# Optimization experiments

Measured on AMD Instinct MI355X. Metric: run time of the kernel, lower is better.

The kernel has to match this reference:

```python
import jax, jax.numpy as jnp
import numpy as np

B, N, E, D, H = 8, 5000, 160000, 64, 128  # batch, nodes, edges, gnn hidden, head hidden


def _w(key, shape, scale=0.05):
    return jax.random.normal(key, shape, jnp.float32) * scale


def setup_inputs() -> dict:
    key = jax.random.key(0)
    ks = jax.random.split(key, 24)
    inp = {
        "x": jax.random.normal(ks[0], (B, N), jnp.float32),
        "edges": jax.random.randint(ks[1], (E, 2), 0, N, dtype=jnp.int32),
        "emb": _w(ks[2], (N, D)),
        # conv1: prepare FFN (2 layers, no bias, elu), update FFN (2 layers, bias)
        "c1_pw1": _w(ks[3], (D, D)), "c1_pw2": _w(ks[4], (D, D)),
        "c1_uw1": _w(ks[5], (2 * D, D)), "c1_ub1": jnp.zeros((D,), jnp.float32),
        "c1_uw2": _w(ks[6], (D, D)), "c1_ub2": jnp.zeros((D,), jnp.float32),
        # conv2
        "c2_pw1": _w(ks[7], (D, D)), "c2_pw2": _w(ks[8], (D, D)),
        "c2_uw1": _w(ks[9], (2 * D, D)), "c2_ub1": jnp.zeros((D,), jnp.float32),
        "c2_uw2": _w(ks[10], (D, D)), "c2_ub2": jnp.zeros((D,), jnp.float32),
        # TARnet prob heads: flatten -> Dense(H, elu) -> Dense(2) (mu, log_sigma)
        "w0a": _w(ks[11], (N * D, H), 0.005), "b0a": jnp.zeros((H,), jnp.float32),
        "w0b": _w(ks[12], (H, 2)), "b0b": jnp.zeros((2,), jnp.float32),
        "w1a": _w(ks[13], (N * D, H), 0.005), "b1a": jnp.zeros((H,), jnp.float32),
        "w1b": _w(ks[14], (H, 2)), "b1b": jnp.zeros((2,), jnp.float32),
    }
    return inp


def _graph_conv(h, edges, pw1, pw2, uw1, ub1, uw2, ub2):
    # h: [B, N, D]; edges: [E, 2] (parent, node)
    parents = jnp.take(h, edges[:, 0], axis=1)            # [B, E, D] gather
    m = jax.nn.elu(parents @ pw1)                          # prepare FFN (no bias)
    m = jax.nn.elu(m @ pw2)
    agg = jnp.zeros_like(h).at[:, edges[:, 1]].add(m)      # unsorted_segment_sum -> [B, N, D]
    hcat = jnp.concatenate([h, agg], axis=-1)              # combination_type='concat'
    u = jax.nn.elu(hcat @ uw1 + ub1)                       # update FFN
    return u @ uw2 + ub2                                   # final_activation=None


def reference(x, edges, emb,
              c1_pw1, c1_pw2, c1_uw1, c1_ub1, c1_uw2, c1_ub2,
              c2_pw1, c2_pw2, c2_uw1, c2_ub1, c2_uw2, c2_ub2,
              w0a, b0a, w0b, b0b, w1a, b1a, w1b, b1b):
    # node features scale learned per-node embeddings -> [B, N, D]
    h = x[:, :, None] * emb[None, :, :]
    h = _graph_conv(h, edges, c1_pw1, c1_pw2, c1_uw1, c1_ub1, c1_uw2, c1_ub2)
    h = _graph_conv(h, edges, c2_pw1, c2_pw2, c2_uw1, c2_ub1, c2_uw2, c2_ub2)
    phi = h.reshape(h.shape[0], -1)                        # flatten [B, N*D]
    y0 = jax.nn.elu(phi @ w0a + b0a) @ w0b + b0b           # [B, 2] (mu, log_sigma)
    y1 = jax.nn.elu(phi @ w1a + b1a) @ w1b + b1b           # [B, 2]
    return jnp.concatenate([y0, y1], axis=1)               # [B, 4]
```

## Files before the change

### kernel.cpp

```cpp
#include <hip/hip_runtime.h>


constexpr int B = 8, N = 5000, E = 160000, D = 64, H = 128;
constexpr int BN = B * N;
constexpr int ND = N * D;
constexpr long BND = (long)BN * D;
constexpr int KC = 320;
constexpr int NIT = KC / 8;
constexpr int XB = ND / KC;

using f32x4 = __attribute__((ext_vector_type(4))) float;

__device__ __forceinline__ float elu_f(float x) {
    return x > 0.0f ? x : __expf(x) - 1.0f;
}

__device__ __forceinline__ void g2lds16(const float* g, float* l) {
    __builtin_amdgcn_global_load_lds(
        (const __attribute__((address_space(1))) void*)g,
        (__attribute__((address_space(3))) void*)l, 16, 0, 0);
}

__global__ __launch_bounds__(256) void k_count(const int* __restrict__ edges,
                                               int* __restrict__ cnt) {
    int i = blockIdx.x * 256 + threadIdx.x;
    if (i < E) atomicAdd(&cnt[edges[2 * i + 1]], 1);
}

__global__ __launch_bounds__(256) void k_scan(const int* __restrict__ cnt,
                                              int* __restrict__ offs) {
    __shared__ int part[256];
    int t = threadIdx.x;
    const int CH = 20;
    int base = t * CH;
    int s = 0;
    for (int i = 0; i < CH; ++i) { int idx = base + i; if (idx < N) s += cnt[idx]; }
    part[t] = s;
    __syncthreads();
    for (int off = 1; off < 256; off <<= 1) {
        int add = (t >= off) ? part[t - off] : 0;
        __syncthreads();
        part[t] += add;
        __syncthreads();
    }
    int run = part[t] - s;
    for (int i = 0; i < CH; ++i) {
        int idx = base + i;
        if (idx < N) { offs[idx] = run; run += cnt[idx]; }
    }
    if (t == 255) offs[N] = run;
}

__global__ __launch_bounds__(256) void k_fill(const int* __restrict__ edges,
                                              const int* __restrict__ offs,
                                              int* __restrict__ cursor,
                                              int* __restrict__ elist) {
    int i = blockIdx.x * 256 + threadIdx.x;
    if (i < E) {
        int child = edges[2 * i + 1];
        int pos = offs[child] + atomicAdd(&cursor[child], 1);
        elist[pos] = edges[2 * i];
    }
}

__global__ __launch_bounds__(512) void k_prepare(const float* __restrict__ xsrc,
                                                 const float* __restrict__ emb,
                                                 const float* __restrict__ hin,
                                                 const float* __restrict__ W1,
                                                 const float* __restrict__ W2,
                                                 float* __restrict__ M,
                                                 float* __restrict__ hwt) {
    __shared__ float sW1[64 * 64];
    __shared__ float sP[128 * 65];
    int t = threadIdx.x;
    int r0 = blockIdx.x * 128;
    for (int i = t; i < 4096; i += 512) sW1[i] = W1[i];
    if (xsrc) {
        for (int i = t; i < 128 * 64; i += 512) {
            int r = i >> 6, c = i & 63;
            int row = r0 + r;
            float v = 0.0f;
            if (row < BN) {
                int n = row % N;
                v = xsrc[row] * emb[n * 64 + c];
                hwt[(long)row * 64 + c] = v;
            }
            sP[r * 65 + c] = v;
        }
    } else {
        for (int i = t; i < 128 * 64; i += 512) {
            int r = i >> 6, c = i & 63;
            int row = r0 + r;
            sP[r * 65 + c] = (row < BN) ? hin[(long)row * 64 + c] : 0.0f;
        }
    }
    __syncthreads();

    int cg = t & 15, rg = t >> 4;
    float acc[4][4] = {};
    #pragma unroll 4
    for (int k = 0; k < 64; ++k) {
        float a[4];
        #pragma unroll
        for (int i = 0; i < 4; ++i) a[i] = sP[(rg * 4 + i) * 65 + k];
        float4 bb = *reinterpret_cast<const float4*>(&sW1[k * 64 + cg * 4]);
        #pragma unroll
        for (int i = 0; i < 4; ++i) {
            acc[i][0] += a[i] * bb.x; acc[i][1] += a[i] * bb.y;
            acc[i][2] += a[i] * bb.z; acc[i][3] += a[i] * bb.w;
        }
    }
    __syncthreads();
    #pragma unroll
    for (int i = 0; i < 4; ++i)
        #pragma unroll
        for (int j = 0; j < 4; ++j)
            sP[(rg * 4 + i) * 65 + cg * 4 + j] = elu_f(acc[i][j]);
    __syncthreads();

    float acc2[4][4] = {};
    #pragma unroll 4
    for (int k = 0; k < 64; ++k) {
        float a[4];
        #pragma unroll
        for (int i = 0; i < 4; ++i) a[i] = sP[(rg * 4 + i) * 65 + k];
        float4 bb = *reinterpret_cast<const float4*>(&W2[k * 64 + cg * 4]);
        #pragma unroll
        for (int i = 0; i < 4; ++i) {
            acc2[i][0] += a[i] * bb.x; acc2[i][1] += a[i] * bb.y;
            acc2[i][2] += a[i] * bb.z; acc2[i][3] += a[i] * bb.w;
        }
    }
    #pragma unroll
    for (int i = 0; i < 4; ++i) {
        int row = r0 + rg * 4 + i;
        if (row < BN) {
            float4 o = make_float4(elu_f(acc2[i][0]), elu_f(acc2[i][1]),
                                   elu_f(acc2[i][2]), elu_f(acc2[i][3]));
            *reinterpret_cast<float4*>(&M[(long)row * 64 + cg * 4]) = o;
        }
    }
}

template <int PREP>
__global__ __launch_bounds__(512, 8) void k_conv(const float* __restrict__ h,
                                                 const float* __restrict__ M,
                                                 const int* __restrict__ offs,
                                                 const int* __restrict__ elist,
                                                 const float* __restrict__ W1u,
                                                 const float* __restrict__ b1u,
                                                 const float* __restrict__ W2u,
                                                 const float* __restrict__ b2u,
                                                 float* __restrict__ hout,
                                                 const float* __restrict__ W1p,
                                                 const float* __restrict__ W2p,
                                                 float* __restrict__ Mout) {
    __shared__ float sP[64 * 129];
    int t = threadIdx.x;
    long r0 = (long)blockIdx.x * 64;

    for (int s = t; s < 64 * 16; s += 512) {
        int r = s >> 4, c4 = s & 15;
        float4 v = *reinterpret_cast<const float4*>(&h[(r0 + r) * 64 + c4 * 4]);
        int base = r * 129 + c4 * 4;
        sP[base + 0] = v.x; sP[base + 1] = v.y;
        sP[base + 2] = v.z; sP[base + 3] = v.w;
    }
    {
        int wv = t >> 6, lane = t & 63;
        int h4 = lane & 15, le = lane >> 4;
        for (int rr = 0; rr < 8; ++rr) {
            int r = wv * 8 + rr;
            long row = r0 + r;
            int b = (int)(row / N);
            int n = (int)(row - (long)b * N);
            int e0 = offs[n], e1 = offs[n + 1];
            const float* Mb = M + (long)b * ND;
            float4 a = make_float4(0.f, 0.f, 0.f, 0.f);
            float4 a2 = make_float4(0.f, 0.f, 0.f, 0.f);
            int e = e0 + le;
            for (; e + 4 < e1; e += 8) {
                int p1 = elist[e];
                int p2 = elist[e + 4];
                float4 v1 = *reinterpret_cast<const float4*>(&Mb[(long)p1 * 64 + h4 * 4]);
                float4 v2 = *reinterpret_cast<const float4*>(&Mb[(long)p2 * 64 + h4 * 4]);
                a.x += v1.x; a.y += v1.y; a.z += v1.z; a.w += v1.w;
                a2.x += v2.x; a2.y += v2.y; a2.z += v2.z; a2.w += v2.w;
            }
            if (e < e1) {
                int p = elist[e];
                float4 v = *reinterpret_cast<const float4*>(&Mb[(long)p * 64 + h4 * 4]);
                a.x += v.x; a.y += v.y; a.z += v.z; a.w += v.w;
            }
            a.x += a2.x; a.y += a2.y; a.z += a2.z; a.w += a2.w;
            #pragma unroll
            for (int m = 16; m <= 32; m <<= 1) {
                a.x += __shfl_xor(a.x, m);
                a.y += __shfl_xor(a.y, m);
                a.z += __shfl_xor(a.z, m);
                a.w += __shfl_xor(a.w, m);
            }
            if (le == 0) {
                int base = r * 129 + 64 + h4 * 4;
                sP[base + 0] = a.x; sP[base + 1] = a.y;
                sP[base + 2] = a.z; sP[base + 3] = a.w;
            }
        }
    }
    __syncthreads();

    int cg = t & 15, rg = t >> 4;
    float acc[2][4] = {};
    #pragma unroll 4
    for (int k = 0; k < 128; ++k) {
        float a0 = sP[(rg * 2 + 0) * 129 + k];
        float a1 = sP[(rg * 2 + 1) * 129 + k];
        float4 bb = *reinterpret_cast<const float4*>(&W1u[k * 64 + cg * 4]);
        acc[0][0] += a0 * bb.x; acc[0][1] += a0 * bb.y; acc[0][2] += a0 * bb.z; acc[0][3] += a0 * bb.w;
        acc[1][0] += a1 * bb.x; acc[1][1] += a1 * bb.y; acc[1][2] += a1 * bb.z; acc[1][3] += a1 * bb.w;
    }
    float4 bv1 = *reinterpret_cast<const float4*>(&b1u[cg * 4]);
    __syncthreads();
    #pragma unroll
    for (int i = 0; i < 2; ++i) {
        int base = (rg * 2 + i) * 129 + cg * 4;
        sP[base + 0] = elu_f(acc[i][0] + bv1.x);
        sP[base + 1] = elu_f(acc[i][1] + bv1.y);
        sP[base + 2] = elu_f(acc[i][2] + bv1.z);
        sP[base + 3] = elu_f(acc[i][3] + bv1.w);
    }
    __syncthreads();

    float acc2[2][4] = {};
    #pragma unroll 4
    for (int k = 0; k < 64; ++k) {
        float a0 = sP[(rg * 2 + 0) * 129 + k];
        float a1 = sP[(rg * 2 + 1) * 129 + k];
        float4 bb = *reinterpret_cast<const float4*>(&W2u[k * 64 + cg * 4]);
        acc2[0][0] += a0 * bb.x; acc2[0][1] += a0 * bb.y; acc2[0][2] += a0 * bb.z; acc2[0][3] += a0 * bb.w;
        acc2[1][0] += a1 * bb.x; acc2[1][1] += a1 * bb.y; acc2[1][2] += a1 * bb.z; acc2[1][3] += a1 * bb.w;
    }
    float4 bv2 = *reinterpret_cast<const float4*>(&b2u[cg * 4]);
    #pragma unroll
    for (int i = 0; i < 2; ++i) {
        float4 o = make_float4(acc2[i][0] + bv2.x, acc2[i][1] + bv2.y,
                               acc2[i][2] + bv2.z, acc2[i][3] + bv2.w);
        *reinterpret_cast<float4*>(&hout[(r0 + rg * 2 + i) * 64 + cg * 4]) = o;
        if (PREP) {
            int base = (rg * 2 + i) * 129 + 64 + cg * 4;
            sP[base + 0] = o.x; sP[base + 1] = o.y;
            sP[base + 2] = o.z; sP[base + 3] = o.w;
        }
    }

    if (PREP) {
        __syncthreads();
        float acc3[2][4] = {};
        #pragma unroll 4
        for (int k = 0; k < 64; ++k) {
            float a0 = sP[(rg * 2 + 0) * 129 + 64 + k];
            float a1 = sP[(rg * 2 + 1) * 129 + 64 + k];
            float4 bb = *reinterpret_cast<const float4*>(&W1p[k * 64 + cg * 4]);
            acc3[0][0] += a0 * bb.x; acc3[0][1] += a0 * bb.y; acc3[0][2] += a0 * bb.z; acc3[0][3] += a0 * bb.w;
            acc3[1][0] += a1 * bb.x; acc3[1][1] += a1 * bb.y; acc3[1][2] += a1 * bb.z; acc3[1][3] += a1 * bb.w;
        }
        #pragma unroll
        for (int i = 0; i < 2; ++i) {
            int base = (rg * 2 + i) * 129 + cg * 4;
            sP[base + 0] = elu_f(acc3[i][0]);
            sP[base + 1] = elu_f(acc3[i][1]);
            sP[base + 2] = elu_f(acc3[i][2]);
            sP[base + 3] = elu_f(acc3[i][3]);
        }
        __syncthreads();
        float acc4[2][4] = {};
        #pragma unroll 4
        for (int k = 0; k < 64; ++k) {
            float a0 = sP[(rg * 2 + 0) * 129 + k];
            float a1 = sP[(rg * 2 + 1) * 129 + k];
            float4 bb = *reinterpret_cast<const float4*>(&W2p[k * 64 + cg * 4]);
            acc4[0][0] += a0 * bb.x; acc4[0][1] += a0 * bb.y; acc4[0][2] += a0 * bb.z; acc4[0][3] += a0 * bb.w;
            acc4[1][0] += a1 * bb.x; acc4[1][1] += a1 * bb.y; acc4[1][2] += a1 * bb.z; acc4[1][3] += a1 * bb.w;
        }
        #pragma unroll
        for (int i = 0; i < 2; ++i) {
            float4 o = make_float4(elu_f(acc4[i][0]), elu_f(acc4[i][1]),
                                   elu_f(acc4[i][2]), elu_f(acc4[i][3]));
            *reinterpret_cast<float4*>(&Mout[(r0 + rg * 2 + i) * 64 + cg * 4]) = o;
        }
    }
}

__global__ __launch_bounds__(256) void k_head(const float* __restrict__ phi,
                                              const float* __restrict__ wa,
                                              float* __restrict__ part) {
    __shared__ float smem[4 * 32 * 33];
    __shared__ __align__(16) float wb[8][1024];
    int t = threadIdx.x;
    int k0 = blockIdx.x * KC;

    #pragma unroll
    for (int b = 0; b < 8; ++b)
        for (int kk = t; kk < KC; kk += 256)
            smem[b * KC + kk] = phi[(long)b * ND + k0 + kk];
    __syncthreads();

    int w = t >> 6, l = t & 63;
    int h4 = l & 31, kh = l >> 5;
    int kl = w * 2 + kh;
    const float* wp = wa + (long)(k0 + kl) * H + h4 * 4;

    float4 acc[8];
    #pragma unroll
    for (int b = 0; b < 8; ++b) acc[b] = make_float4(0.f, 0.f, 0.f, 0.f);

    unsigned my_off =
        (unsigned)(size_t)(__attribute__((address_space(3))) float*)&wb[0][0]
        + (unsigned)t * 16u;

    const float* wq = wp;
    #pragma unroll
    for (int j = 0; j < 8; ++j) {
        g2lds16(wq, &wb[j][w * 256]);
        wq += 8 * H;
    }

#define STEP(I, CNT, OFF, RE)                                              \
    {                                                                      \
        asm volatile("s_waitcnt vmcnt(" #CNT ")" ::: "memory");            \
        __builtin_amdgcn_sched_barrier(0);                                 \
        f32x4 w4;                                                          \
        asm volatile("ds_read_b128 %0, %1 offset:" #OFF                    \
                     : "=v"(w4) : "v"(my_off));                            \
        float pv[8];                                                       \
        _Pragma("unroll")                                                  \
        for (int b = 0; b < 8; ++b)                                        \
            pv[b] = smem[b * KC + (I) * 8 + kl];                           \
        asm volatile("s_waitcnt lgkmcnt(0)" ::: "memory");                 \
        __builtin_amdgcn_sched_barrier(0);                                 \
        _Pragma("unroll")                                                  \
        for (int b = 0; b < 8; ++b) {                                      \
            acc[b].x += pv[b] * w4.x; acc[b].y += pv[b] * w4.y;            \
            acc[b].z += pv[b] * w4.z; acc[b].w += pv[b] * w4.w;            \
        }                                                                  \
        if (RE) {                                                          \
            g2lds16(wq, &wb[(I) & 7][w * 256]);                            \
            wq += 8 * H;                                                   \
        }                                                                  \
    }

#define ROUND8(BASE, RE)                                                   \
    STEP(BASE + 0, 7, 0,     RE) STEP(BASE + 1, 7, 4096,  RE)              \
    STEP(BASE + 2, 7, 8192,  RE) STEP(BASE + 3, 7, 12288, RE)              \
    STEP(BASE + 4, 7, 16384, RE) STEP(BASE + 5, 7, 20480, RE)              \
    STEP(BASE + 6, 7, 24576, RE) STEP(BASE + 7, 7, 28672, RE)

    ROUND8(0, 1) ROUND8(8, 1) ROUND8(16, 1) ROUND8(24, 1)
    STEP(32, 7, 0,     0) STEP(33, 6, 4096,  0)
    STEP(34, 5, 8192,  0) STEP(35, 4, 12288, 0)
    STEP(36, 3, 16384, 0) STEP(37, 2, 20480, 0)
    STEP(38, 1, 24576, 0) STEP(39, 0, 28672, 0)
#undef ROUND8
#undef STEP

    #pragma unroll
    for (int b = 0; b < 8; ++b) {
        acc[b].x += __shfl_xor(acc[b].x, 32);
        acc[b].y += __shfl_xor(acc[b].y, 32);
        acc[b].z += __shfl_xor(acc[b].z, 32);
        acc[b].w += __shfl_xor(acc[b].w, 32);
    }
    __syncthreads();
    if (kh == 0) {
        int base = (w * 32 + h4) * 33;
        #pragma unroll
        for (int b = 0; b < 8; ++b) {
            smem[base + b * 4 + 0] = acc[b].x;
            smem[base + b * 4 + 1] = acc[b].y;
            smem[base + b * 4 + 2] = acc[b].z;
            smem[base + b * 4 + 3] = acc[b].w;
        }
    }
    __syncthreads();

    int h4r = t & 31, br = t >> 5;
    float s0 = 0.f, s1 = 0.f, s2 = 0.f, s3 = 0.f;
    #pragma unroll
    for (int wv = 0; wv < 4; ++wv) {
        int idx = (wv * 32 + h4r) * 33 + br * 4;
        s0 += smem[idx + 0]; s1 += smem[idx + 1];
        s2 += smem[idx + 2]; s3 += smem[idx + 3];
    }
    float* pb = part + (long)blockIdx.x * 1024;
    *reinterpret_cast<float4*>(&pb[br * H + h4r * 4]) =
        make_float4(s0, s1, s2, s3);
}

__global__ __launch_bounds__(256) void k_reduce(const float* __restrict__ part,
                                                float* __restrict__ hidden) {
    int idx = blockIdx.x * 256 + threadIdx.x;
    int c = blockIdx.y;
    int y = idx >> 10, j = idx & 1023;
    const float* p = part + (long)y * XB * 1024 + j;
    int x0 = (XB * c) >> 4, x1 = (XB * (c + 1)) >> 4;
    float s0 = 0.f, s1 = 0.f, s2 = 0.f, s3 = 0.f;
    int x = x0;
    for (; x + 3 < x1; x += 4) {
        s0 += p[(long)(x + 0) * 1024];
        s1 += p[(long)(x + 1) * 1024];
        s2 += p[(long)(x + 2) * 1024];
        s3 += p[(long)(x + 3) * 1024];
    }
    for (; x < x1; ++x) s0 += p[(long)x * 1024];
    unsafeAtomicAdd(&hidden[y * 1024 + j], s0 + s1 + s2 + s3);
}

__global__ __launch_bounds__(64) void k_final(const float* __restrict__ hidden,
                                              const float* __restrict__ b0a,
                                              const float* __restrict__ w0b,
                                              const float* __restrict__ b0b,
                                              const float* __restrict__ b1a,
                                              const float* __restrict__ w1b,
                                              const float* __restrict__ b1b,
                                              float* __restrict__ out) {
    int t = threadIdx.x;
    if (t >= 32) return;
    int head = t >> 4, b = (t >> 1) & 7, j = t & 1;
    const float* hid = hidden + head * (8 * H) + b * H;
    const float* ba = head ? b1a : b0a;
    const float* wb = head ? w1b : w0b;
    const float* bb = head ? b1b : b0b;
    float acc = 0.0f;
    for (int hh = 0; hh < H; ++hh)
        acc += elu_f(hid[hh] + ba[hh]) * wb[hh * 2 + j];
    out[b * 4 + head * 2 + j] = acc + bb[j];
}

extern "C" void kernel_launch(void* const* d_in, const int* in_sizes, int n_in,
                              void* d_out, int out_size, void* d_ws, size_t ws_size,
                              hipStream_t stream) {
    const float* x      = (const float*)d_in[0];
    const int*   edges  = (const int*)d_in[1];
    const float* emb    = (const float*)d_in[2];
    const float* c1_pw1 = (const float*)d_in[3];
    const float* c1_pw2 = (const float*)d_in[4];
    const float* c1_uw1 = (const float*)d_in[5];
    const float* c1_ub1 = (const float*)d_in[6];
    const float* c1_uw2 = (const float*)d_in[7];
    const float* c1_ub2 = (const float*)d_in[8];
    const float* c2_pw1 = (const float*)d_in[9];
    const float* c2_pw2 = (const float*)d_in[10];
    const float* c2_uw1 = (const float*)d_in[11];
    const float* c2_ub1 = (const float*)d_in[12];
    const float* c2_uw2 = (const float*)d_in[13];
    const float* c2_ub2 = (const float*)d_in[14];
    const float* w0a    = (const float*)d_in[15];
    const float* b0a    = (const float*)d_in[16];
    const float* w0b    = (const float*)d_in[17];
    const float* b0b    = (const float*)d_in[18];
    const float* w1a    = (const float*)d_in[19];
    const float* b1a    = (const float*)d_in[20];
    const float* w1b    = (const float*)d_in[21];
    const float* b1b    = (const float*)d_in[22];
    float* out = (float*)d_out;

    float* hA     = (float*)d_ws;
    float* hB     = hA + BND;
    float* Mu     = hB + BND;
    float* M2     = Mu + BND;
    float* hidden = M2 + BND;
    int* cnt      = (int*)(hidden + 2048);
    int* cursor   = cnt + N;
    int* offs     = cursor + N;
    int* elist    = offs + N + 1;
    float* part   = Mu;

    hipMemsetAsync(hidden, 0, (2048 + 2 * N) * sizeof(float), stream);

    k_count<<<(E + 255) / 256, 256, 0, stream>>>(edges, cnt);
    k_scan<<<1, 256, 0, stream>>>(cnt, offs);
    k_fill<<<(E + 255) / 256, 256, 0, stream>>>(edges, offs, cursor, elist);

    k_prepare<<<(BN + 127) / 128, 512, 0, stream>>>(x, emb, nullptr, c1_pw1, c1_pw2, Mu, hA);
    k_conv<1><<<BN / 64, 512, 0, stream>>>(hA, Mu, offs, elist,
                                           c1_uw1, c1_ub1, c1_uw2, c1_ub2, hB,
                                           c2_pw1, c2_pw2, M2);
    k_conv<0><<<BN / 64, 512, 0, stream>>>(hB, M2, offs, elist,
                                           c2_uw1, c2_ub1, c2_uw2, c2_ub2, hA,
                                           nullptr, nullptr, nullptr);

    k_head<<<XB, 256, 0, stream>>>(hA, w0a, part);
    k_head<<<XB, 256, 0, stream>>>(hA, w1a, part + (long)XB * 1024);
    k_reduce<<<dim3(8, 16), 256, 0, stream>>>(part, hidden);
    k_final<<<1, 64, 0, stream>>>(hidden, b0a, w0b, b0b, b1a, w1b, b1b, out);
}
```

Measured before the change: 639.4 us.

## Store messages node-major across batch and gather all batches per edge

Messages M are now stored as [N][B][D], so one parent's messages for all 8 batch items form a contiguous 2KB block. Each conv block now handles 8 nodes across all batches, with one wavefront per node reading every parent block once with fully coalesced float4 loads. Edge offsets become wave-uniform through readfirstlane. The aim is to cut repeated elist reads and scattered 256B gathers across batches, at the cost of h reads and writes being strided across batch rows.

```diff
diff --git a/kernel.cpp b/kernel.cpp
--- a/kernel.cpp
+++ b/kernel.cpp
@@ -65,7 +65,6 @@
 
 __global__ __launch_bounds__(512) void k_prepare(const float* __restrict__ xsrc,
                                                  const float* __restrict__ emb,
-                                                 const float* __restrict__ hin,
                                                  const float* __restrict__ W1,
                                                  const float* __restrict__ W2,
                                                  float* __restrict__ M,
@@ -75,24 +74,16 @@
     int t = threadIdx.x;
     int r0 = blockIdx.x * 128;
     for (int i = t; i < 4096; i += 512) sW1[i] = W1[i];
-    if (xsrc) {
-        for (int i = t; i < 128 * 64; i += 512) {
-            int r = i >> 6, c = i & 63;
-            int row = r0 + r;
-            float v = 0.0f;
-            if (row < BN) {
-                int n = row % N;
-                v = xsrc[row] * emb[n * 64 + c];
-                hwt[(long)row * 64 + c] = v;
-            }
-            sP[r * 65 + c] = v;
-        }
-    } else {
-        for (int i = t; i < 128 * 64; i += 512) {
-            int r = i >> 6, c = i & 63;
-            int row = r0 + r;
-            sP[r * 65 + c] = (row < BN) ? hin[(long)row * 64 + c] : 0.0f;
-        }
+    for (int i = t; i < 128 * 64; i += 512) {
+        int r = i >> 6, c = i & 63;
+        int row = r0 + r;
+        float v = 0.0f;
+        if (row < BN) {
+            int n = row % N;
+            v = xsrc[row] * emb[n * 64 + c];
+            hwt[(long)row * 64 + c] = v;
+        }
+        sP[r * 65 + c] = v;
     }
     __syncthreads();
 
@@ -135,9 +126,11 @@
     for (int i = 0; i < 4; ++i) {
         int row = r0 + rg * 4 + i;
         if (row < BN) {
+            int b = row / N;
+            int n = row - b * N;
             float4 o = make_float4(elu_f(acc2[i][0]), elu_f(acc2[i][1]),
                                    elu_f(acc2[i][2]), elu_f(acc2[i][3]));
-            *reinterpret_cast<float4*>(&M[(long)row * 64 + cg * 4]) = o;
+            *reinterpret_cast<float4*>(&M[((long)n * 8 + b) * 64 + cg * 4]) = o;
         }
     }
 }
@@ -157,55 +150,56 @@
                                                  float* __restrict__ Mout) {
     __shared__ float sP[64 * 129];
     int t = threadIdx.x;
-    long r0 = (long)blockIdx.x * 64;
-
-    for (int s = t; s < 64 * 16; s += 512) {
-        int r = s >> 4, c4 = s & 15;
-        float4 v = *reinterpret_cast<const float4*>(&h[(r0 + r) * 64 + c4 * 4]);
-        int base = r * 129 + c4 * 4;
+    int n0 = blockIdx.x * 8;
+
+    #pragma unroll
+    for (int q = 0; q < 2; ++q) {
+        int s = t + q * 512;
+        int lr = s >> 4, c4 = s & 15;
+        int nl = lr >> 3, b = lr & 7;
+        long grow = (long)b * N + (n0 + nl);
+        float4 v = *reinterpret_cast<const float4*>(&h[grow * 64 + c4 * 4]);
+        int base = lr * 129 + c4 * 4;
         sP[base + 0] = v.x; sP[base + 1] = v.y;
         sP[base + 2] = v.z; sP[base + 3] = v.w;
     }
     {
-        int wv = t >> 6, lane = t & 63;
-        int h4 = lane & 15, le = lane >> 4;
-        for (int rr = 0; rr < 8; ++rr) {
-            int r = wv * 8 + rr;
-            long row = r0 + r;
-            int b = (int)(row / N);
-            int n = (int)(row - (long)b * N);
-            int e0 = offs[n], e1 = offs[n + 1];
-            const float* Mb = M + (long)b * ND;
-            float4 a = make_float4(0.f, 0.f, 0.f, 0.f);
-            float4 a2 = make_float4(0.f, 0.f, 0.f, 0.f);
-            int e = e0 + le;
-            for (; e + 4 < e1; e += 8) {
-                int p1 = elist[e];
-                int p2 = elist[e + 4];
-                float4 v1 = *reinterpret_cast<const float4*>(&Mb[(long)p1 * 64 + h4 * 4]);
-                float4 v2 = *reinterpret_cast<const float4*>(&Mb[(long)p2 * 64 + h4 * 4]);
-                a.x += v1.x; a.y += v1.y; a.z += v1.z; a.w += v1.w;
-                a2.x += v2.x; a2.y += v2.y; a2.z += v2.z; a2.w += v2.w;
-            }
-            if (e < e1) {
-                int p = elist[e];
-                float4 v = *reinterpret_cast<const float4*>(&Mb[(long)p * 64 + h4 * 4]);
-                a.x += v.x; a.y += v.y; a.z += v.z; a.w += v.w;
-            }
-            a.x += a2.x; a.y += a2.y; a.z += a2.z; a.w += a2.w;
-            #pragma unroll
-            for (int m = 16; m <= 32; m <<= 1) {
-                a.x += __shfl_xor(a.x, m);
-                a.y += __shfl_xor(a.y, m);
-                a.z += __shfl_xor(a.z, m);
-                a.w += __shfl_xor(a.w, m);
-            }
-            if (le == 0) {
-                int base = r * 129 + 64 + h4 * 4;
-                sP[base + 0] = a.x; sP[base + 1] = a.y;
-                sP[base + 2] = a.z; sP[base + 3] = a.w;
-            }
-        }
+        int wv = t >> 6, l = t & 63;
+        int n = n0 + wv;
+        int e0 = __builtin_amdgcn_readfirstlane(offs[n]);
+        int e1 = __builtin_amdgcn_readfirstlane(offs[n + 1]);
+        float4 a1 = make_float4(0.f, 0.f, 0.f, 0.f);
+        float4 a2 = make_float4(0.f, 0.f, 0.f, 0.f);
+        float4 a3 = make_float4(0.f, 0.f, 0.f, 0.f);
+        float4 a4 = make_float4(0.f, 0.f, 0.f, 0.f);
+        int e = e0;
+        for (; e + 1 < e1; e += 2) {
+            int p1 = elist[e], p2 = elist[e + 1];
+            const float4* q1 = reinterpret_cast<const float4*>(M + (long)p1 * 512);
+            const float4* q2 = reinterpret_cast<const float4*>(M + (long)p2 * 512);
+            float4 v1 = q1[l], v2 = q1[64 + l];
+            float4 v3 = q2[l], v4 = q2[64 + l];
+            a1.x += v1.x; a1.y += v1.y; a1.z += v1.z; a1.w += v1.w;
+            a2.x += v2.x; a2.y += v2.y; a2.z += v2.z; a2.w += v2.w;
+            a3.x += v3.x; a3.y += v3.y; a3.z += v3.z; a3.w += v3.w;
+            a4.x += v4.x; a4.y += v4.y; a4.z += v4.z; a4.w += v4.w;
+        }
+        if (e < e1) {
+            int p = elist[e];
+            const float4* q = reinterpret_cast<const float4*>(M + (long)p * 512);
+            float4 v1 = q[l], v2 = q[64 + l];
+            a1.x += v1.x; a1.y += v1.y; a1.z += v1.z; a1.w += v1.w;
+            a2.x += v2.x; a2.y += v2.y; a2.z += v2.z; a2.w += v2.w;
+        }
+        a1.x += a3.x; a1.y += a3.y; a1.z += a3.z; a1.w += a3.w;
+        a2.x += a4.x; a2.y += a4.y; a2.z += a4.z; a2.w += a4.w;
+        int c4 = l & 15, br = l >> 4;
+        int base1 = (wv * 8 + br) * 129 + 64 + c4 * 4;
+        int base2 = (wv * 8 + 4 + br) * 129 + 64 + c4 * 4;
+        sP[base1 + 0] = a1.x; sP[base1 + 1] = a1.y;
+        sP[base1 + 2] = a1.z; sP[base1 + 3] = a1.w;
+        sP[base2 + 0] = a2.x; sP[base2 + 1] = a2.y;
+        sP[base2 + 2] = a2.z; sP[base2 + 3] = a2.w;
     }
     __syncthreads();
 
@@ -243,11 +237,14 @@
     float4 bv2 = *reinterpret_cast<const float4*>(&b2u[cg * 4]);
     #pragma unroll
     for (int i = 0; i < 2; ++i) {
+        int lr = rg * 2 + i;
+        int nl = lr >> 3, b = lr & 7;
         float4 o = make_float4(acc2[i][0] + bv2.x, acc2[i][1] + bv2.y,
                                acc2[i][2] + bv2.z, acc2[i][3] + bv2.w);
-        *reinterpret_cast<float4*>(&hout[(r0 + rg * 2 + i) * 64 + cg * 4]) = o;
+        *reinterpret_cast<float4*>(
+            &hout[((long)b * N + (n0 + nl)) * 64 + cg * 4]) = o;
         if (PREP) {
-            int base = (rg * 2 + i) * 129 + 64 + cg * 4;
+            int base = lr * 129 + 64 + cg * 4;
             sP[base + 0] = o.x; sP[base + 1] = o.y;
             sP[base + 2] = o.z; sP[base + 3] = o.w;
         }
@@ -284,9 +281,12 @@
         }
         #pragma unroll
         for (int i = 0; i < 2; ++i) {
+            int lr = rg * 2 + i;
+            int nl = lr >> 3, b = lr & 7;
             float4 o = make_float4(elu_f(acc4[i][0]), elu_f(acc4[i][1]),
                                    elu_f(acc4[i][2]), elu_f(acc4[i][3]));
-            *reinterpret_cast<float4*>(&Mout[(r0 + rg * 2 + i) * 64 + cg * 4]) = o;
+            *reinterpret_cast<float4*>(
+                &Mout[((long)(n0 + nl) * 8 + b) * 64 + cg * 4]) = o;
         }
     }
 }
@@ -481,13 +481,13 @@
     k_scan<<<1, 256, 0, stream>>>(cnt, offs);
     k_fill<<<(E + 255) / 256, 256, 0, stream>>>(edges, offs, cursor, elist);
 
-    k_prepare<<<(BN + 127) / 128, 512, 0, stream>>>(x, emb, nullptr, c1_pw1, c1_pw2, Mu, hA);
-    k_conv<1><<<BN / 64, 512, 0, stream>>>(hA, Mu, offs, elist,
-                                           c1_uw1, c1_ub1, c1_uw2, c1_ub2, hB,
-                                           c2_pw1, c2_pw2, M2);
-    k_conv<0><<<BN / 64, 512, 0, stream>>>(hB, M2, offs, elist,
-                                           c2_uw1, c2_ub1, c2_uw2, c2_ub2, hA,
-                                           nullptr, nullptr, nullptr);
+    k_prepare<<<(BN + 127) / 128, 512, 0, stream>>>(x, emb, c1_pw1, c1_pw2, Mu, hA);
+    k_conv<1><<<N / 8, 512, 0, stream>>>(hA, Mu, offs, elist,
+                                         c1_uw1, c1_ub1, c1_uw2, c1_ub2, hB,
+                                         c2_pw1, c2_pw2, M2);
+    k_conv<0><<<N / 8, 512, 0, stream>>>(hB, M2, offs, elist,
+                                         c2_uw1, c2_ub1, c2_uw2, c2_ub2, hA,
+                                         nullptr, nullptr, nullptr);
 
     k_head<<<XB, 256, 0, stream>>>(hA, w0a, part);
     k_head<<<XB, 256, 0, stream>>>(hA, w1a, part + (long)XB * 1024);
```

Measured after the change: 626.7 us. 1.02x faster.
